# Kernel optimization log

Hardware: AMD Instinct MI355X
Metric: run time of the kernel (lower is better)

## Reference

```python
import jax, jax.numpy as jnp
import numpy as np

N_NODES = 100000
N_EDGES = 1600000
N_GRAPHS = 64
IN_CH, HID_CH, OUT_CH, N_CLS = 128, 128, 64, 2


def setup_inputs() -> dict:
    key = jax.random.key(0)
    ks = jax.random.split(key, 8)
    x = jax.random.normal(ks[0], (N_NODES, IN_CH), dtype=jnp.float32)
    edge_index = jax.random.randint(ks[1], (2, N_EDGES), 0, N_NODES)
    batch = jnp.sort(jax.random.randint(ks[2], (N_NODES,), 0, N_GRAPHS))
    glorot = lambda k, shp: jax.random.normal(k, shp, dtype=jnp.float32) / np.float32(np.sqrt(shp[0]))
    return {
        "x": x, "edge_index": edge_index, "batch": batch,
        "W1": glorot(ks[3], (IN_CH, HID_CH)), "b1": jnp.zeros((HID_CH,), jnp.float32),
        "W2": glorot(ks[4], (HID_CH, HID_CH)), "b2": jnp.zeros((HID_CH,), jnp.float32),
        "W3": glorot(ks[5], (HID_CH, OUT_CH)), "b3": jnp.zeros((OUT_CH,), jnp.float32),
        "Wfc": glorot(ks[6], (OUT_CH, N_CLS)), "bfc": jnp.zeros((N_CLS,), jnp.float32),
    }


def gcn_conv(x, src, dst, W, b):
    """PyG GCNConv: add self-loops, D^{-1/2} (A+I) D^{-1/2} (x W) + b."""
    n = x.shape[0]
    h = x @ W  # [N, out]
    # degree with self-loops: 1 + in-degree at dst
    deg = jnp.ones((n,), h.dtype).at[dst].add(1.0)
    dinv = jax.lax.rsqrt(deg)  # deg >= 1 always (self-loop)
    norm = dinv[src] * dinv[dst]  # [E]
    agg = jnp.zeros_like(h).at[dst].add(h[src] * norm[:, None])
    agg = agg + h * (dinv * dinv)[:, None]  # self-loop messages
    return agg + b


def global_mean_pool(x, batch, num_graphs):
    s = jax.ops.segment_sum(x, batch, num_segments=num_graphs)
    cnt = jax.ops.segment_sum(jnp.ones((x.shape[0],), x.dtype), batch, num_segments=num_graphs)
    return s / jnp.maximum(cnt, 1.0)[:, None]


def reference(x, edge_index, batch, W1, b1, W2, b2, W3, b3, Wfc, bfc):
    src, dst = edge_index[0], edge_index[1]
    h = jax.nn.relu(gcn_conv(x, src, dst, W1, b1))   # dropout p=0.0 (eval) -> identity
    h = jax.nn.relu(gcn_conv(h, src, dst, W2, b2))
    h = gcn_conv(h, src, dst, W3, b3)
    g = global_mean_pool(h, batch, N_GRAPHS)          # [G, OUT_CH]
    return g @ Wfc + bfc                              # [G, N_CLS]
```

## Files before the change

kernel.cpp:

```cpp
#include <hip/hip_runtime.h>
#include <hip/hip_bf16.h>


#define THREADS 256
#define BSHIFT 9
#define BSIZE 512

typedef __attribute__((ext_vector_type(8))) short short8;
typedef __attribute__((ext_vector_type(16))) float floatx16;

__device__ __forceinline__ unsigned f2bf(float f) {
    unsigned u = __float_as_uint(f);
    return (u + 0x7fffu + ((u >> 16) & 1u)) >> 16;
}

__device__ __forceinline__ void bf8_acc(uint4 v, float* ac) {
    ac[0] += __uint_as_float(v.x << 16);
    ac[1] += __uint_as_float(v.x & 0xffff0000u);
    ac[2] += __uint_as_float(v.y << 16);
    ac[3] += __uint_as_float(v.y & 0xffff0000u);
    ac[4] += __uint_as_float(v.z << 16);
    ac[5] += __uint_as_float(v.z & 0xffff0000u);
    ac[6] += __uint_as_float(v.w << 16);
    ac[7] += __uint_as_float(v.w & 0xffff0000u);
}


__global__ __launch_bounds__(512) void zero_btotal(int* btotal, int nbuck) {
    if ((int)threadIdx.x < nbuck) btotal[threadIdx.x] = 0;
}

__global__ __launch_bounds__(THREADS) void zero_f32(float* p, int n) {
    int i = blockIdx.x * THREADS + threadIdx.x;
    if (i < n) p[i] = 0.0f;
}

__global__ __launch_bounds__(THREADS) void bucket_count(const int* __restrict__ dst,
                                                        int* __restrict__ btotal,
                                                        int E, int nbuck) {
    __shared__ int cnt[BSIZE];
    for (int i = threadIdx.x; i < nbuck; i += THREADS) cnt[i] = 0;
    __syncthreads();
    for (int e = blockIdx.x * THREADS + threadIdx.x; e < E; e += gridDim.x * THREADS)
        atomicAdd(&cnt[dst[e] >> BSHIFT], 1);
    __syncthreads();
    for (int i = threadIdx.x; i < nbuck; i += THREADS) {
        int c = cnt[i];
        if (c) atomicAdd(&btotal[i], c);
    }
}

__global__ __launch_bounds__(512) void bucket_scan(const int* __restrict__ btotal,
                                                   int* __restrict__ bbase,
                                                   int* __restrict__ bcursor,
                                                   int nbuck, int E) {
    __shared__ int lds[512];
    int t = threadIdx.x;
    int v = (t < nbuck) ? btotal[t] : 0;
    lds[t] = v;
    __syncthreads();
    for (int off = 1; off < 512; off <<= 1) {
        int tv = (t >= off) ? lds[t - off] : 0;
        __syncthreads();
        lds[t] += tv;
        __syncthreads();
    }
    if (t < nbuck) {
        int excl = lds[t] - v;
        bbase[t] = excl;
        bcursor[t] = excl;
    }
    if (t == 0) bbase[nbuck] = E;
}

__global__ __launch_bounds__(THREADS) void bucket_scatter(const int* __restrict__ src,
                                                          const int* __restrict__ dst,
                                                          int* __restrict__ bcursor,
                                                          int2* __restrict__ pairs, int E) {
    __shared__ int cnt[BSIZE];
    __shared__ int base[BSIZE];
    for (int i = threadIdx.x; i < BSIZE; i += THREADS) cnt[i] = 0;
    __syncthreads();
    int e0 = blockIdx.x * 2048;
    int myb[8], myrank[8], mysrc[8], mydst[8];
#pragma unroll
    for (int j = 0; j < 8; ++j) {
        int e = e0 + j * THREADS + threadIdx.x;
        myb[j] = -1;
        if (e < E) {
            int d = dst[e];
            mysrc[j] = src[e];
            mydst[j] = d;
            myb[j] = d >> BSHIFT;
            myrank[j] = atomicAdd(&cnt[myb[j]], 1);
        }
    }
    __syncthreads();
    for (int i = threadIdx.x; i < BSIZE; i += THREADS) {
        int c = cnt[i];
        base[i] = c ? atomicAdd(&bcursor[i], c) : 0;
    }
    __syncthreads();
#pragma unroll
    for (int j = 0; j < 8; ++j)
        if (myb[j] >= 0) pairs[(size_t)base[myb[j]] + myrank[j]] = make_int2(mysrc[j], mydst[j]);
}

__global__ __launch_bounds__(512) void bucket_fill(const int2* __restrict__ pairs,
                                                   const int* __restrict__ bbase,
                                                   int* __restrict__ row_start,
                                                   float* __restrict__ dinv,
                                                   int* __restrict__ esrc,
                                                   int N, int E, int nbuck) {
    __shared__ int cnt[BSIZE];
    __shared__ int scn[BSIZE];
    int b = blockIdx.x, t = threadIdx.x;
    int s = bbase[b], e = bbase[b + 1];
    cnt[t] = 0;
    __syncthreads();
    for (int i = s + t; i < e; i += 512) atomicAdd(&cnt[pairs[i].y & (BSIZE - 1)], 1);
    __syncthreads();
    int v = cnt[t];
    scn[t] = v;
    __syncthreads();
    for (int off = 1; off < 512; off <<= 1) {
        int tv = (t >= off) ? scn[t - off] : 0;
        __syncthreads();
        scn[t] += tv;
        __syncthreads();
    }
    int excl = scn[t] - v;
    int g = (b << BSHIFT) + t;
    if (g < N) {
        row_start[g] = s + excl;
        dinv[g] = rsqrtf(1.0f + (float)v);
    }
    if (b == nbuck - 1 && t == 0) row_start[N] = E;
    scn[t] = excl;
    __syncthreads();
    for (int i = s + t; i < e; i += 512) {
        int2 p = pairs[i];
        int r = atomicAdd(&scn[p.y & (BSIZE - 1)], 1);
        esrc[s + r] = p.x;
    }
}

__global__ __launch_bounds__(THREADS) void prep_wt(const float* __restrict__ W,
                                                   uint4* __restrict__ Wtp, int C) {
    int idx = blockIdx.x * THREADS + threadIdx.x;
    if (idx >= C * 16) return;
    int c = idx >> 4, ch = idx & 15;
    unsigned r[8];
#pragma unroll
    for (int j = 0; j < 8; ++j) r[j] = f2bf(W[(size_t)(ch * 8 + j) * C + c]);
    uint4 o;
    o.x = r[0] | (r[1] << 16);
    o.y = r[2] | (r[3] << 16);
    o.z = r[4] | (r[5] << 16);
    o.w = r[6] | (r[7] << 16);
    Wtp[idx] = o;
}

template <int C, bool IN_F32>
__global__ __launch_bounds__(THREADS) void gemm_mfma(const void* __restrict__ Xin,
                                                     const uint4* __restrict__ Wt,
                                                     const float* __restrict__ dinv,
                                                     uint4* __restrict__ Hs, int n) {
    __shared__ __align__(16) char lds_raw[16384 + C * 256];
    int row0 = blockIdx.x * 64;
    int maxr = n - row0;
    if (maxr > 64) maxr = 64;
    int tid = threadIdx.x;

    if (IN_F32) {
        const float* X = (const float*)Xin;
        for (int idx = tid; idx < 1024; idx += THREADS) {
            int r = idx >> 4, c = idx & 15;
            uint4 o = make_uint4(0, 0, 0, 0);
            if (r < maxr) {
                const float* p = X + (size_t)(row0 + r) * 128 + c * 8;
                float4 a = *(const float4*)p;
                float4 b = *(const float4*)(p + 4);
                o.x = f2bf(a.x) | (f2bf(a.y) << 16);
                o.y = f2bf(a.z) | (f2bf(a.w) << 16);
                o.z = f2bf(b.x) | (f2bf(b.y) << 16);
                o.w = f2bf(b.z) | (f2bf(b.w) << 16);
            }
            *(uint4*)(lds_raw + r * 256 + ((c ^ (r & 7)) * 16)) = o;
        }
    } else {
        const uint4* X = (const uint4*)Xin;
        for (int idx = tid; idx < 1024; idx += THREADS) {
            int r = idx >> 4, c = idx & 15;
            uint4 o = (r < maxr) ? X[(size_t)(row0 + r) * 16 + c] : make_uint4(0, 0, 0, 0);
            *(uint4*)(lds_raw + r * 256 + ((c ^ (r & 7)) * 16)) = o;
        }
    }
    for (int idx = tid; idx < C * 16; idx += THREADS) {
        int cc = idx >> 4, c = idx & 15;
        *(uint4*)(lds_raw + 16384 + cc * 256 + ((c ^ (cc & 7)) * 16)) = Wt[idx];
    }
    __syncthreads();

    int wave = tid >> 6, lane = tid & 63;
    int l31 = lane & 31, half = lane >> 5;
    constexpr int MT = (C == 128) ? 2 : 1;
    int nt = wave & 1;
    int mt0 = (C == 128) ? ((wave >> 1) * 2) : (wave >> 1);
    floatx16 acc[MT];
#pragma unroll
    for (int t = 0; t < MT; ++t)
#pragma unroll
        for (int q = 0; q < 16; ++q) acc[t][q] = 0.0f;

    int xrow = nt * 32 + l31;
    const char* xbase = lds_raw + xrow * 256;
    int xsw = xrow & 7;
    const char* wbase[MT];
    int wsw[MT];
#pragma unroll
    for (int t = 0; t < MT; ++t) {
        int wrow = (mt0 + t) * 32 + l31;
        wbase[t] = lds_raw + 16384 + wrow * 256;
        wsw[t] = wrow & 7;
    }
#pragma unroll
    for (int kt = 0; kt < 8; ++kt) {
        int chunk = kt * 2 + half;
        short8 xf = *(const short8*)(xbase + ((chunk ^ xsw) * 16));
#pragma unroll
        for (int t = 0; t < MT; ++t) {
            short8 wf = *(const short8*)(wbase[t] + ((chunk ^ wsw[t]) * 16));
            acc[t] = __builtin_amdgcn_mfma_f32_32x32x16_bf16(wf, xf, acc[t], 0, 0, 0);
        }
    }
    __syncthreads();

    int node = nt * 32 + l31;
    float dv = (node < maxr) ? dinv[row0 + node] : 0.0f;
    char* outb = lds_raw;
#pragma unroll
    for (int t = 0; t < MT; ++t) {
        int cbase = (mt0 + t) * 32;
#pragma unroll
        for (int q = 0; q < 4; ++q) {
            unsigned p0 = f2bf(acc[t][q * 4 + 0] * dv) | (f2bf(acc[t][q * 4 + 1] * dv) << 16);
            unsigned p1 = f2bf(acc[t][q * 4 + 2] * dv) | (f2bf(acc[t][q * 4 + 3] * dv) << 16);
            int chunk = (cbase >> 3) + q;
            uint2 pk = make_uint2(p0, p1);
            *(uint2*)(outb + node * (C * 2) + ((chunk ^ (node & 7)) * 16) + half * 8) = pk;
        }
    }
    __syncthreads();
    constexpr int RCH = C / 8;
    for (int idx = tid; idx < maxr * RCH; idx += THREADS) {
        int r = idx / RCH, c = idx % RCH;
        uint4 v = *(const uint4*)(outb + r * (C * 2) + ((c ^ (r & 7)) * 16));
        Hs[(size_t)(row0 + r) * RCH + c] = v;
    }
}

template <int C, bool RELU>
__global__ __launch_bounds__(THREADS) void agg_kernel(const unsigned* __restrict__ Hs,
                                                      const int* __restrict__ row_start,
                                                      const int* __restrict__ esrc,
                                                      const float* __restrict__ dinv,
                                                      const float* __restrict__ bias,
                                                      unsigned* __restrict__ out, int n) {
    constexpr int LPN = C / 8;
    constexpr int NPB = THREADS / LPN;
    int node = blockIdx.x * NPB + threadIdx.x / LPN;
    int lane = threadIdx.x % LPN;
    if (node >= n) return;
    const uint4* H4 = (const uint4*)Hs;
    float di = dinv[node];
    int s = row_start[node], e = row_start[node + 1];
    float ac[8] = {0, 0, 0, 0, 0, 0, 0, 0};
    bf8_acc(H4[(size_t)node * LPN + lane], ac);
    int i = s;
    for (; i + 8 <= e; i += 8) {
        int s0 = esrc[i], s1 = esrc[i + 1], s2 = esrc[i + 2], s3 = esrc[i + 3];
        int s4 = esrc[i + 4], s5 = esrc[i + 5], s6 = esrc[i + 6], s7 = esrc[i + 7];
        uint4 v0 = H4[(size_t)s0 * LPN + lane];
        uint4 v1 = H4[(size_t)s1 * LPN + lane];
        uint4 v2 = H4[(size_t)s2 * LPN + lane];
        uint4 v3 = H4[(size_t)s3 * LPN + lane];
        uint4 v4 = H4[(size_t)s4 * LPN + lane];
        uint4 v5 = H4[(size_t)s5 * LPN + lane];
        uint4 v6 = H4[(size_t)s6 * LPN + lane];
        uint4 v7 = H4[(size_t)s7 * LPN + lane];
        bf8_acc(v0, ac); bf8_acc(v1, ac); bf8_acc(v2, ac); bf8_acc(v3, ac);
        bf8_acc(v4, ac); bf8_acc(v5, ac); bf8_acc(v6, ac); bf8_acc(v7, ac);
    }
    for (; i + 4 <= e; i += 4) {
        int s0 = esrc[i], s1 = esrc[i + 1], s2 = esrc[i + 2], s3 = esrc[i + 3];
        uint4 v0 = H4[(size_t)s0 * LPN + lane];
        uint4 v1 = H4[(size_t)s1 * LPN + lane];
        uint4 v2 = H4[(size_t)s2 * LPN + lane];
        uint4 v3 = H4[(size_t)s3 * LPN + lane];
        bf8_acc(v0, ac); bf8_acc(v1, ac); bf8_acc(v2, ac); bf8_acc(v3, ac);
    }
    for (; i < e; ++i) bf8_acc(H4[(size_t)esrc[i] * LPN + lane], ac);

    float4 b0 = ((const float4*)bias)[lane * 2];
    float4 b1 = ((const float4*)bias)[lane * 2 + 1];
    float o_[8];
    o_[0] = fmaf(di, ac[0], b0.x); o_[1] = fmaf(di, ac[1], b0.y);
    o_[2] = fmaf(di, ac[2], b0.z); o_[3] = fmaf(di, ac[3], b0.w);
    o_[4] = fmaf(di, ac[4], b1.x); o_[5] = fmaf(di, ac[5], b1.y);
    o_[6] = fmaf(di, ac[6], b1.z); o_[7] = fmaf(di, ac[7], b1.w);
    if (RELU) {
#pragma unroll
        for (int j = 0; j < 8; ++j) o_[j] = fmaxf(o_[j], 0.0f);
    }
    uint4 o;
    o.x = f2bf(o_[0]) | (f2bf(o_[1]) << 16);
    o.y = f2bf(o_[2]) | (f2bf(o_[3]) << 16);
    o.z = f2bf(o_[4]) | (f2bf(o_[5]) << 16);
    o.w = f2bf(o_[6]) | (f2bf(o_[7]) << 16);
    ((uint4*)out)[(size_t)node * LPN + lane] = o;
}

#define PCHUNK 512

__global__ __launch_bounds__(THREADS) void pool1_kernel(const unsigned* __restrict__ H3,
                                                        const int* __restrict__ batch, int n,
                                                        float* __restrict__ gsum) {
    int base = blockIdx.x * PCHUNK;
    int lane = threadIdx.x & 7;
    int sub = threadIdx.x >> 3;
    const uint4* H4 = (const uint4*)H3;
    float ac[8] = {0, 0, 0, 0, 0, 0, 0, 0};
    int cur_g = -1;
    int end = min(base + PCHUNK, n);
    for (int i = base + sub; i < end; i += 32) {
        int g = batch[i];
        if (g != cur_g) {
            if (cur_g >= 0) {
                float* p = gsum + cur_g * 64 + lane * 8;
#pragma unroll
                for (int j = 0; j < 8; ++j) atomicAdd(p + j, ac[j]);
#pragma unroll
                for (int j = 0; j < 8; ++j) ac[j] = 0.0f;
            }
            cur_g = g;
        }
        bf8_acc(H4[(size_t)i * 8 + lane], ac);
    }
    if (cur_g >= 0) {
        float* p = gsum + cur_g * 64 + lane * 8;
#pragma unroll
        for (int j = 0; j < 8; ++j) atomicAdd(p + j, ac[j]);
    }
}

__device__ __forceinline__ int dev_lower_bound(const int* a, int n, int key) {
    int lo = 0, hi = n;
    while (lo < hi) {
        int mid = (lo + hi) >> 1;
        if (a[mid] < key) lo = mid + 1;
        else hi = mid;
    }
    return lo;
}

__global__ __launch_bounds__(128) void finalize_fc(const float* __restrict__ gsum,
                                                   const int* __restrict__ batch, int n,
                                                   const float* __restrict__ Wfc,
                                                   const float* __restrict__ bfc,
                                                   float* __restrict__ out) {
    __shared__ float gm[64 * 64];
    __shared__ float cnt[64];
    int t = threadIdx.x;
    if (t < 64)
        cnt[t] = (float)(dev_lower_bound(batch, n, t + 1) - dev_lower_bound(batch, n, t));
    __syncthreads();
    for (int i = t; i < 64 * 64; i += 128) gm[i] = gsum[i] / fmaxf(cnt[i >> 6], 1.0f);
    __syncthreads();
    int g = t >> 1, cls = t & 1;
    float acc = bfc[cls];
    for (int c = 0; c < 64; ++c) acc = fmaf(gm[g * 64 + c], Wfc[c * 2 + cls], acc);
    out[g * 2 + cls] = acc;
}

extern "C" void kernel_launch(void* const* d_in, const int* in_sizes, int n_in,
                              void* d_out, int out_size, void* d_ws, size_t ws_size,
                              hipStream_t stream) {
    const float* x    = (const float*)d_in[0];
    const int*   ei   = (const int*)d_in[1];
    const int*   batch= (const int*)d_in[2];
    const float* W1   = (const float*)d_in[3];
    const float* b1   = (const float*)d_in[4];
    const float* W2   = (const float*)d_in[5];
    const float* b2   = (const float*)d_in[6];
    const float* W3   = (const float*)d_in[7];
    const float* b3   = (const float*)d_in[8];
    const float* Wfc  = (const float*)d_in[9];
    const float* bfc  = (const float*)d_in[10];
    float* out = (float*)d_out;

    const int N = in_sizes[2];
    const int E = in_sizes[1] / 2;
    const int* esrc_in = ei;
    const int* edst_in = ei + E;
    const int nbuck = (N + BSIZE - 1) >> BSHIFT;

    unsigned* bufA      = (unsigned*)d_ws;
    unsigned* bufH      = bufA + (size_t)N * 128;
    int2*     pairs     = (int2*)(bufH + (size_t)N * 64);
    int*      esrc      = (int*)(pairs + E);
    int*      row_start = esrc + E;
    float*    dinv      = (float*)(row_start + N + 1);
    int*      btotal    = (int*)(dinv + N);
    int*      bbase     = btotal + 512;
    int*      bcursor   = bbase + 513;
    float*    gsum      = (float*)(bcursor + 512);
    uint4*    Wt1       = (uint4*)(gsum + 64 * 64);
    uint4*    Wt2       = Wt1 + 2048;
    uint4*    Wt3       = Wt2 + 2048;

    prep_wt<<<8, THREADS, 0, stream>>>(W1, Wt1, 128);
    prep_wt<<<8, THREADS, 0, stream>>>(W2, Wt2, 128);
    prep_wt<<<4, THREADS, 0, stream>>>(W3, Wt3, 64);
    zero_btotal<<<1, 512, 0, stream>>>(btotal, nbuck);
    zero_f32<<<16, THREADS, 0, stream>>>(gsum, 64 * 64);
    bucket_count<<<512, THREADS, 0, stream>>>(edst_in, btotal, E, nbuck);
    bucket_scan<<<1, 512, 0, stream>>>(btotal, bbase, bcursor, nbuck, E);
    bucket_scatter<<<(E + 2047) / 2048, THREADS, 0, stream>>>(esrc_in, edst_in, bcursor, pairs, E);
    bucket_fill<<<nbuck, 512, 0, stream>>>(pairs, bbase, row_start, dinv, esrc, N, E, nbuck);

    const int GB = (N + 63) / 64;

    gemm_mfma<128, true><<<GB, THREADS, 0, stream>>>(x, Wt1, dinv, (uint4*)bufH, N);
    agg_kernel<128, true><<<(N + 15) / 16, THREADS, 0, stream>>>(bufH, row_start, esrc, dinv, b1, bufA, N);

    gemm_mfma<128, false><<<GB, THREADS, 0, stream>>>(bufA, Wt2, dinv, (uint4*)bufH, N);
    agg_kernel<128, true><<<(N + 15) / 16, THREADS, 0, stream>>>(bufH, row_start, esrc, dinv, b2, bufA, N);

    gemm_mfma<64, false><<<GB, THREADS, 0, stream>>>(bufA, Wt3, dinv, (uint4*)bufH, N);
    agg_kernel<64, false><<<(N + 31) / 32, THREADS, 0, stream>>>(bufH, row_start, esrc, dinv, b3, bufA, N);

    pool1_kernel<<<(N + PCHUNK - 1) / PCHUNK, THREADS, 0, stream>>>(bufA, batch, N, gsum);
    finalize_fc<<<1, 128, 0, stream>>>(gsum, batch, N, Wfc, bfc, out);
}
```

Measured before the change: 437.3 us.

## Fuse aggregation with next-layer GEMM, fuse final aggregation with pooling

The layer order is reassociated so each layer first aggregates the pre-scaled features and then multiplies by the weight inside one kernel, with bias, ReLU and the next dinv scaling in the GEMM epilogue. A separate prep kernel converts x to bf16 with dinv scaling. The last layer's aggregation writes straight into per-block shared-memory graph sums for mean pooling, which drops the output buffer and the pool kernel. Zeroing moves to hipMemsetAsync and the three weight-prep launches merge into one. Weights are now read from global memory per MFMA instead of being staged in LDS, and each fused block does a serial gather over 64 nodes before its GEMM.

```diff
diff --git a/kernel.cpp b/kernel.cpp
--- a/kernel.cpp
+++ b/kernel.cpp
@@ -25,15 +25,6 @@
     ac[7] += __uint_as_float(v.w & 0xffff0000u);
 }
 
-
-__global__ __launch_bounds__(512) void zero_btotal(int* btotal, int nbuck) {
-    if ((int)threadIdx.x < nbuck) btotal[threadIdx.x] = 0;
-}
-
-__global__ __launch_bounds__(THREADS) void zero_f32(float* p, int n) {
-    int i = blockIdx.x * THREADS + threadIdx.x;
-    if (i < n) p[i] = 0.0f;
-}
 
 __global__ __launch_bounds__(THREADS) void bucket_count(const int* __restrict__ dst,
                                                         int* __restrict__ btotal,
@@ -145,11 +136,8 @@
     }
 }
 
-__global__ __launch_bounds__(THREADS) void prep_wt(const float* __restrict__ W,
-                                                   uint4* __restrict__ Wtp, int C) {
-    int idx = blockIdx.x * THREADS + threadIdx.x;
-    if (idx >= C * 16) return;
-    int c = idx >> 4, ch = idx & 15;
+__device__ __forceinline__ void wt_pack(const float* W, uint4* Wtp, int C, int li) {
+    int c = li >> 4, ch = li & 15;
     unsigned r[8];
 #pragma unroll
     for (int j = 0; j < 8; ++j) r[j] = f2bf(W[(size_t)(ch * 8 + j) * C + c]);
@@ -158,79 +146,111 @@
     o.y = r[2] | (r[3] << 16);
     o.z = r[4] | (r[5] << 16);
     o.w = r[6] | (r[7] << 16);
-    Wtp[idx] = o;
-}
-
-template <int C, bool IN_F32>
-__global__ __launch_bounds__(THREADS) void gemm_mfma(const void* __restrict__ Xin,
-                                                     const uint4* __restrict__ Wt,
-                                                     const float* __restrict__ dinv,
-                                                     uint4* __restrict__ Hs, int n) {
-    __shared__ __align__(16) char lds_raw[16384 + C * 256];
+    Wtp[li] = o;
+}
+
+__global__ __launch_bounds__(THREADS) void prep_wt_all(const float* __restrict__ W1,
+                                                       const float* __restrict__ W2,
+                                                       const float* __restrict__ W3,
+                                                       uint4* __restrict__ Wt1,
+                                                       uint4* __restrict__ Wt2,
+                                                       uint4* __restrict__ Wt3) {
+    int idx = blockIdx.x * THREADS + threadIdx.x;
+    if (idx < 2048) wt_pack(W1, Wt1, 128, idx);
+    else if (idx < 4096) wt_pack(W2, Wt2, 128, idx - 2048);
+    else if (idx < 5120) wt_pack(W3, Wt3, 64, idx - 4096);
+}
+
+__global__ __launch_bounds__(THREADS) void prep_x(const float* __restrict__ x,
+                                                  const float* __restrict__ dinv,
+                                                  uint4* __restrict__ Z, int n) {
+    int idx = blockIdx.x * THREADS + threadIdx.x;
+    if (idx >= n * 16) return;
+    int r = idx >> 4, c = idx & 15;
+    float dv = dinv[r];
+    const float* p = x + (size_t)r * 128 + c * 8;
+    float4 a = *(const float4*)p;
+    float4 b = *(const float4*)(p + 4);
+    uint4 o;
+    o.x = f2bf(a.x * dv) | (f2bf(a.y * dv) << 16);
+    o.y = f2bf(a.z * dv) | (f2bf(a.w * dv) << 16);
+    o.z = f2bf(b.x * dv) | (f2bf(b.y * dv) << 16);
+    o.w = f2bf(b.z * dv) | (f2bf(b.w * dv) << 16);
+    Z[idx] = o;
+}
+
+__global__ __launch_bounds__(THREADS) void fused_layer(const uint4* __restrict__ Z,
+                                                       const uint4* __restrict__ Wt,
+                                                       const int* __restrict__ row_start,
+                                                       const int* __restrict__ esrc,
+                                                       const float* __restrict__ dinv,
+                                                       const float* __restrict__ bias,
+                                                       uint4* __restrict__ out, int n) {
+    __shared__ __align__(16) uint4 ldsX[64 * 16];
     int row0 = blockIdx.x * 64;
     int maxr = n - row0;
     if (maxr > 64) maxr = 64;
     int tid = threadIdx.x;
-
-    if (IN_F32) {
-        const float* X = (const float*)Xin;
-        for (int idx = tid; idx < 1024; idx += THREADS) {
-            int r = idx >> 4, c = idx & 15;
-            uint4 o = make_uint4(0, 0, 0, 0);
-            if (r < maxr) {
-                const float* p = X + (size_t)(row0 + r) * 128 + c * 8;
-                float4 a = *(const float4*)p;
-                float4 b = *(const float4*)(p + 4);
-                o.x = f2bf(a.x) | (f2bf(a.y) << 16);
-                o.y = f2bf(a.z) | (f2bf(a.w) << 16);
-                o.z = f2bf(b.x) | (f2bf(b.y) << 16);
-                o.w = f2bf(b.z) | (f2bf(b.w) << 16);
-            }
-            *(uint4*)(lds_raw + r * 256 + ((c ^ (r & 7)) * 16)) = o;
-        }
-    } else {
-        const uint4* X = (const uint4*)Xin;
-        for (int idx = tid; idx < 1024; idx += THREADS) {
-            int r = idx >> 4, c = idx & 15;
-            uint4 o = (r < maxr) ? X[(size_t)(row0 + r) * 16 + c] : make_uint4(0, 0, 0, 0);
-            *(uint4*)(lds_raw + r * 256 + ((c ^ (r & 7)) * 16)) = o;
-        }
-    }
-    for (int idx = tid; idx < C * 16; idx += THREADS) {
-        int cc = idx >> 4, c = idx & 15;
-        *(uint4*)(lds_raw + 16384 + cc * 256 + ((c ^ (cc & 7)) * 16)) = Wt[idx];
-    }
-    __syncthreads();
-
-    int wave = tid >> 6, lane = tid & 63;
-    int l31 = lane & 31, half = lane >> 5;
-    constexpr int MT = (C == 128) ? 2 : 1;
-    int nt = wave & 1;
-    int mt0 = (C == 128) ? ((wave >> 1) * 2) : (wave >> 1);
-    floatx16 acc[MT];
-#pragma unroll
-    for (int t = 0; t < MT; ++t)
+    int lane = tid & 15, grp = tid >> 4;
+
+    for (int round = 0; round < 4; ++round) {
+        int r = round * 16 + grp;
+        int node = row0 + r;
+        int nd = (node < n) ? node : (n - 1);
+        float ac[8] = {0, 0, 0, 0, 0, 0, 0, 0};
+        bf8_acc(Z[(size_t)nd * 16 + lane], ac);
+        int s = row_start[nd], e = row_start[nd + 1];
+        int i = s;
+        for (; i + 8 <= e; i += 8) {
+            int s0 = esrc[i], s1 = esrc[i + 1], s2 = esrc[i + 2], s3 = esrc[i + 3];
+            int s4 = esrc[i + 4], s5 = esrc[i + 5], s6 = esrc[i + 6], s7 = esrc[i + 7];
+            uint4 v0 = Z[(size_t)s0 * 16 + lane];
+            uint4 v1 = Z[(size_t)s1 * 16 + lane];
+            uint4 v2 = Z[(size_t)s2 * 16 + lane];
+            uint4 v3 = Z[(size_t)s3 * 16 + lane];
+            uint4 v4 = Z[(size_t)s4 * 16 + lane];
+            uint4 v5 = Z[(size_t)s5 * 16 + lane];
+            uint4 v6 = Z[(size_t)s6 * 16 + lane];
+            uint4 v7 = Z[(size_t)s7 * 16 + lane];
+            bf8_acc(v0, ac); bf8_acc(v1, ac); bf8_acc(v2, ac); bf8_acc(v3, ac);
+            bf8_acc(v4, ac); bf8_acc(v5, ac); bf8_acc(v6, ac); bf8_acc(v7, ac);
+        }
+        for (; i + 4 <= e; i += 4) {
+            int s0 = esrc[i], s1 = esrc[i + 1], s2 = esrc[i + 2], s3 = esrc[i + 3];
+            uint4 v0 = Z[(size_t)s0 * 16 + lane];
+            uint4 v1 = Z[(size_t)s1 * 16 + lane];
+            uint4 v2 = Z[(size_t)s2 * 16 + lane];
+            uint4 v3 = Z[(size_t)s3 * 16 + lane];
+            bf8_acc(v0, ac); bf8_acc(v1, ac); bf8_acc(v2, ac); bf8_acc(v3, ac);
+        }
+        for (; i < e; ++i) bf8_acc(Z[(size_t)esrc[i] * 16 + lane], ac);
+        float dv = dinv[nd];
+        uint4 o;
+        o.x = f2bf(ac[0] * dv) | (f2bf(ac[1] * dv) << 16);
+        o.y = f2bf(ac[2] * dv) | (f2bf(ac[3] * dv) << 16);
+        o.z = f2bf(ac[4] * dv) | (f2bf(ac[5] * dv) << 16);
+        o.w = f2bf(ac[6] * dv) | (f2bf(ac[7] * dv) << 16);
+        ldsX[r * 16 + (lane ^ (r & 7))] = o;
+    }
+    __syncthreads();
+
+    int l = tid & 63, wv = tid >> 6;
+    int l31 = l & 31, half = l >> 5;
+    int nt = wv & 1, mt0 = (wv >> 1) * 2;
+    floatx16 acc[2];
+#pragma unroll
+    for (int t = 0; t < 2; ++t)
 #pragma unroll
         for (int q = 0; q < 16; ++q) acc[t][q] = 0.0f;
-
-    int xrow = nt * 32 + l31;
-    const char* xbase = lds_raw + xrow * 256;
-    int xsw = xrow & 7;
-    const char* wbase[MT];
-    int wsw[MT];
-#pragma unroll
-    for (int t = 0; t < MT; ++t) {
-        int wrow = (mt0 + t) * 32 + l31;
-        wbase[t] = lds_raw + 16384 + wrow * 256;
-        wsw[t] = wrow & 7;
-    }
+    int xrow = nt * 32 + l31, xsw = xrow & 7;
 #pragma unroll
     for (int kt = 0; kt < 8; ++kt) {
         int chunk = kt * 2 + half;
-        short8 xf = *(const short8*)(xbase + ((chunk ^ xsw) * 16));
-#pragma unroll
-        for (int t = 0; t < MT; ++t) {
-            short8 wf = *(const short8*)(wbase[t] + ((chunk ^ wsw[t]) * 16));
+        short8 xf = *(const short8*)&ldsX[xrow * 16 + (chunk ^ xsw)];
+#pragma unroll
+        for (int t = 0; t < 2; ++t) {
+            int c = (mt0 + t) * 32 + l31;
+            short8 wf = *(const short8*)&Wt[c * 16 + chunk];
             acc[t] = __builtin_amdgcn_mfma_f32_32x32x16_bf16(wf, xf, acc[t], 0, 0, 0);
         }
     }
@@ -238,119 +258,147 @@
 
     int node = nt * 32 + l31;
     float dv = (node < maxr) ? dinv[row0 + node] : 0.0f;
-    char* outb = lds_raw;
-#pragma unroll
-    for (int t = 0; t < MT; ++t) {
-        int cbase = (mt0 + t) * 32;
+    char* outb = (char*)ldsX;
+#pragma unroll
+    for (int t = 0; t < 2; ++t) {
+        int cb = (mt0 + t) * 32;
 #pragma unroll
         for (int q = 0; q < 4; ++q) {
-            unsigned p0 = f2bf(acc[t][q * 4 + 0] * dv) | (f2bf(acc[t][q * 4 + 1] * dv) << 16);
-            unsigned p1 = f2bf(acc[t][q * 4 + 2] * dv) | (f2bf(acc[t][q * 4 + 3] * dv) << 16);
-            int chunk = (cbase >> 3) + q;
-            uint2 pk = make_uint2(p0, p1);
-            *(uint2*)(outb + node * (C * 2) + ((chunk ^ (node & 7)) * 16) + half * 8) = pk;
-        }
-    }
-    __syncthreads();
-    constexpr int RCH = C / 8;
-    for (int idx = tid; idx < maxr * RCH; idx += THREADS) {
-        int r = idx / RCH, c = idx % RCH;
-        uint4 v = *(const uint4*)(outb + r * (C * 2) + ((c ^ (r & 7)) * 16));
-        Hs[(size_t)(row0 + r) * RCH + c] = v;
-    }
-}
-
-template <int C, bool RELU>
-__global__ __launch_bounds__(THREADS) void agg_kernel(const unsigned* __restrict__ Hs,
-                                                      const int* __restrict__ row_start,
-                                                      const int* __restrict__ esrc,
-                                                      const float* __restrict__ dinv,
-                                                      const float* __restrict__ bias,
-                                                      unsigned* __restrict__ out, int n) {
-    constexpr int LPN = C / 8;
-    constexpr int NPB = THREADS / LPN;
-    int node = blockIdx.x * NPB + threadIdx.x / LPN;
-    int lane = threadIdx.x % LPN;
-    if (node >= n) return;
-    const uint4* H4 = (const uint4*)Hs;
-    float di = dinv[node];
-    int s = row_start[node], e = row_start[node + 1];
-    float ac[8] = {0, 0, 0, 0, 0, 0, 0, 0};
-    bf8_acc(H4[(size_t)node * LPN + lane], ac);
-    int i = s;
-    for (; i + 8 <= e; i += 8) {
-        int s0 = esrc[i], s1 = esrc[i + 1], s2 = esrc[i + 2], s3 = esrc[i + 3];
-        int s4 = esrc[i + 4], s5 = esrc[i + 5], s6 = esrc[i + 6], s7 = esrc[i + 7];
-        uint4 v0 = H4[(size_t)s0 * LPN + lane];
-        uint4 v1 = H4[(size_t)s1 * LPN + lane];
-        uint4 v2 = H4[(size_t)s2 * LPN + lane];
-        uint4 v3 = H4[(size_t)s3 * LPN + lane];
-        uint4 v4 = H4[(size_t)s4 * LPN + lane];
-        uint4 v5 = H4[(size_t)s5 * LPN + lane];
-        uint4 v6 = H4[(size_t)s6 * LPN + lane];
-        uint4 v7 = H4[(size_t)s7 * LPN + lane];
-        bf8_acc(v0, ac); bf8_acc(v1, ac); bf8_acc(v2, ac); bf8_acc(v3, ac);
-        bf8_acc(v4, ac); bf8_acc(v5, ac); bf8_acc(v6, ac); bf8_acc(v7, ac);
-    }
-    for (; i + 4 <= e; i += 4) {
-        int s0 = esrc[i], s1 = esrc[i + 1], s2 = esrc[i + 2], s3 = esrc[i + 3];
-        uint4 v0 = H4[(size_t)s0 * LPN + lane];
-        uint4 v1 = H4[(size_t)s1 * LPN + lane];
-        uint4 v2 = H4[(size_t)s2 * LPN + lane];
-        uint4 v3 = H4[(size_t)s3 * LPN + lane];
-        bf8_acc(v0, ac); bf8_acc(v1, ac); bf8_acc(v2, ac); bf8_acc(v3, ac);
-    }
-    for (; i < e; ++i) bf8_acc(H4[(size_t)esrc[i] * LPN + lane], ac);
-
-    float4 b0 = ((const float4*)bias)[lane * 2];
-    float4 b1 = ((const float4*)bias)[lane * 2 + 1];
-    float o_[8];
-    o_[0] = fmaf(di, ac[0], b0.x); o_[1] = fmaf(di, ac[1], b0.y);
-    o_[2] = fmaf(di, ac[2], b0.z); o_[3] = fmaf(di, ac[3], b0.w);
-    o_[4] = fmaf(di, ac[4], b1.x); o_[5] = fmaf(di, ac[5], b1.y);
-    o_[6] = fmaf(di, ac[6], b1.z); o_[7] = fmaf(di, ac[7], b1.w);
-    if (RELU) {
-#pragma unroll
-        for (int j = 0; j < 8; ++j) o_[j] = fmaxf(o_[j], 0.0f);
-    }
-    uint4 o;
-    o.x = f2bf(o_[0]) | (f2bf(o_[1]) << 16);
-    o.y = f2bf(o_[2]) | (f2bf(o_[3]) << 16);
-    o.z = f2bf(o_[4]) | (f2bf(o_[5]) << 16);
-    o.w = f2bf(o_[6]) | (f2bf(o_[7]) << 16);
-    ((uint4*)out)[(size_t)node * LPN + lane] = o;
-}
-
-#define PCHUNK 512
-
-__global__ __launch_bounds__(THREADS) void pool1_kernel(const unsigned* __restrict__ H3,
-                                                        const int* __restrict__ batch, int n,
-                                                        float* __restrict__ gsum) {
-    int base = blockIdx.x * PCHUNK;
-    int lane = threadIdx.x & 7;
-    int sub = threadIdx.x >> 3;
-    const uint4* H4 = (const uint4*)H3;
-    float ac[8] = {0, 0, 0, 0, 0, 0, 0, 0};
-    int cur_g = -1;
-    int end = min(base + PCHUNK, n);
-    for (int i = base + sub; i < end; i += 32) {
-        int g = batch[i];
-        if (g != cur_g) {
-            if (cur_g >= 0) {
-                float* p = gsum + cur_g * 64 + lane * 8;
-#pragma unroll
-                for (int j = 0; j < 8; ++j) atomicAdd(p + j, ac[j]);
-#pragma unroll
-                for (int j = 0; j < 8; ++j) ac[j] = 0.0f;
+            float v[4];
+#pragma unroll
+            for (int m = 0; m < 4; ++m) {
+                int ch = cb + 8 * q + 4 * half + m;
+                float x_ = acc[t][q * 4 + m] + bias[ch];
+                x_ = fmaxf(x_, 0.0f);
+                v[m] = x_ * dv;
             }
-            cur_g = g;
-        }
-        bf8_acc(H4[(size_t)i * 8 + lane], ac);
-    }
-    if (cur_g >= 0) {
-        float* p = gsum + cur_g * 64 + lane * 8;
-#pragma unroll
-        for (int j = 0; j < 8; ++j) atomicAdd(p + j, ac[j]);
+            uint2 pk = make_uint2(f2bf(v[0]) | (f2bf(v[1]) << 16),
+                                  f2bf(v[2]) | (f2bf(v[3]) << 16));
+            int chunk = (cb >> 3) + q;
+            *(uint2*)(outb + node * 256 + ((chunk ^ (node & 7)) * 16) + half * 8) = pk;
+        }
+    }
+    __syncthreads();
+    for (int idx = tid; idx < maxr * 16; idx += THREADS) {
+        int r = idx >> 4, c = idx & 15;
+        out[(size_t)(row0 + r) * 16 + c] = *(uint4*)(outb + r * 256 + ((c ^ (r & 7)) * 16));
+    }
+}
+
+__global__ __launch_bounds__(THREADS) void gemm3(const uint4* __restrict__ Z,
+                                                 const uint4* __restrict__ Wt,
+                                                 uint4* __restrict__ out, int n) {
+    __shared__ __align__(16) uint4 ldsX[64 * 16];
+    int row0 = blockIdx.x * 64;
+    int maxr = n - row0;
+    if (maxr > 64) maxr = 64;
+    int tid = threadIdx.x;
+    for (int idx = tid; idx < 1024; idx += THREADS) {
+        int r = idx >> 4, c = idx & 15;
+        uint4 o = (r < maxr) ? Z[(size_t)(row0 + r) * 16 + c] : make_uint4(0, 0, 0, 0);
+        ldsX[r * 16 + (c ^ (r & 7))] = o;
+    }
+    __syncthreads();
+    int l = tid & 63, wv = tid >> 6;
+    int l31 = l & 31, half = l >> 5;
+    int nt = wv & 1, mt = wv >> 1;
+    floatx16 acc;
+#pragma unroll
+    for (int q = 0; q < 16; ++q) acc[q] = 0.0f;
+    int xrow = nt * 32 + l31, xsw = xrow & 7;
+#pragma unroll
+    for (int kt = 0; kt < 8; ++kt) {
+        int chunk = kt * 2 + half;
+        short8 xf = *(const short8*)&ldsX[xrow * 16 + (chunk ^ xsw)];
+        int c = mt * 32 + l31;
+        short8 wf = *(const short8*)&Wt[c * 16 + chunk];
+        acc = __builtin_amdgcn_mfma_f32_32x32x16_bf16(wf, xf, acc, 0, 0, 0);
+    }
+    __syncthreads();
+    int node = nt * 32 + l31;
+    char* outb = (char*)ldsX;
+    int cb = mt * 32;
+#pragma unroll
+    for (int q = 0; q < 4; ++q) {
+        uint2 pk = make_uint2(f2bf(acc[q * 4 + 0]) | (f2bf(acc[q * 4 + 1]) << 16),
+                              f2bf(acc[q * 4 + 2]) | (f2bf(acc[q * 4 + 3]) << 16));
+        int chunk = (cb >> 3) + q;
+        *(uint2*)(outb + node * 128 + ((chunk ^ (node & 7)) * 16) + half * 8) = pk;
+    }
+    __syncthreads();
+    for (int idx = tid; idx < maxr * 8; idx += THREADS) {
+        int r = idx >> 3, c = idx & 7;
+        out[(size_t)(row0 + r) * 8 + c] = *(uint4*)(outb + r * 128 + ((c ^ (r & 7)) * 16));
+    }
+}
+
+__global__ __launch_bounds__(THREADS) void agg_pool(const uint4* __restrict__ Ps,
+                                                    const int* __restrict__ row_start,
+                                                    const int* __restrict__ esrc,
+                                                    const float* __restrict__ dinv,
+                                                    const float* __restrict__ bias,
+                                                    const int* __restrict__ batch,
+                                                    float* __restrict__ gsum, int n) {
+    __shared__ float gpart[32][65];
+    __shared__ int used[32];
+    int tid = threadIdx.x;
+    int lane = tid & 7, grp = tid >> 3;
+    int node = blockIdx.x * 32 + grp;
+    if (tid < 32) used[tid] = 0;
+    for (int idx = tid; idx < 2048; idx += THREADS) gpart[idx >> 6][idx & 63] = 0.0f;
+    __syncthreads();
+    int gmin = batch[blockIdx.x * 32];
+    if (node < n) {
+        float ac[8] = {0, 0, 0, 0, 0, 0, 0, 0};
+        bf8_acc(Ps[(size_t)node * 8 + lane], ac);
+        int s = row_start[node], e = row_start[node + 1];
+        int i = s;
+        for (; i + 8 <= e; i += 8) {
+            int s0 = esrc[i], s1 = esrc[i + 1], s2 = esrc[i + 2], s3 = esrc[i + 3];
+            int s4 = esrc[i + 4], s5 = esrc[i + 5], s6 = esrc[i + 6], s7 = esrc[i + 7];
+            uint4 v0 = Ps[(size_t)s0 * 8 + lane];
+            uint4 v1 = Ps[(size_t)s1 * 8 + lane];
+            uint4 v2 = Ps[(size_t)s2 * 8 + lane];
+            uint4 v3 = Ps[(size_t)s3 * 8 + lane];
+            uint4 v4 = Ps[(size_t)s4 * 8 + lane];
+            uint4 v5 = Ps[(size_t)s5 * 8 + lane];
+            uint4 v6 = Ps[(size_t)s6 * 8 + lane];
+            uint4 v7 = Ps[(size_t)s7 * 8 + lane];
+            bf8_acc(v0, ac); bf8_acc(v1, ac); bf8_acc(v2, ac); bf8_acc(v3, ac);
+            bf8_acc(v4, ac); bf8_acc(v5, ac); bf8_acc(v6, ac); bf8_acc(v7, ac);
+        }
+        for (; i + 4 <= e; i += 4) {
+            int s0 = esrc[i], s1 = esrc[i + 1], s2 = esrc[i + 2], s3 = esrc[i + 3];
+            uint4 v0 = Ps[(size_t)s0 * 8 + lane];
+            uint4 v1 = Ps[(size_t)s1 * 8 + lane];
+            uint4 v2 = Ps[(size_t)s2 * 8 + lane];
+            uint4 v3 = Ps[(size_t)s3 * 8 + lane];
+            bf8_acc(v0, ac); bf8_acc(v1, ac); bf8_acc(v2, ac); bf8_acc(v3, ac);
+        }
+        for (; i < e; ++i) bf8_acc(Ps[(size_t)esrc[i] * 8 + lane], ac);
+        float dv = dinv[node];
+        float4 b0 = ((const float4*)bias)[lane * 2];
+        float4 b1 = ((const float4*)bias)[lane * 2 + 1];
+        float h[8];
+        h[0] = fmaf(dv, ac[0], b0.x); h[1] = fmaf(dv, ac[1], b0.y);
+        h[2] = fmaf(dv, ac[2], b0.z); h[3] = fmaf(dv, ac[3], b0.w);
+        h[4] = fmaf(dv, ac[4], b1.x); h[5] = fmaf(dv, ac[5], b1.y);
+        h[6] = fmaf(dv, ac[6], b1.z); h[7] = fmaf(dv, ac[7], b1.w);
+        int g = batch[node];
+        int slot = g - gmin;
+        if (slot < 32) {
+            if (lane == 0) used[slot] = 1;
+#pragma unroll
+            for (int j = 0; j < 8; ++j) atomicAdd(&gpart[slot][lane * 8 + j], h[j]);
+        } else {
+#pragma unroll
+            for (int j = 0; j < 8; ++j) atomicAdd(&gsum[(size_t)g * 64 + lane * 8 + j], h[j]);
+        }
+    }
+    __syncthreads();
+    for (int idx = tid; idx < 2048; idx += THREADS) {
+        int s = idx >> 6, ch = idx & 63;
+        if (used[s]) atomicAdd(&gsum[(size_t)(gmin + s) * 64 + ch], gpart[s][ch]);
     }
 }
 
@@ -405,41 +453,36 @@
     const int* edst_in = ei + E;
     const int nbuck = (N + BSIZE - 1) >> BSHIFT;
 
-    unsigned* bufA      = (unsigned*)d_ws;
-    unsigned* bufH      = bufA + (size_t)N * 128;
-    int2*     pairs     = (int2*)(bufH + (size_t)N * 64);
-    int*      esrc      = (int*)(pairs + E);
-    int*      row_start = esrc + E;
-    float*    dinv      = (float*)(row_start + N + 1);
-    int*      btotal    = (int*)(dinv + N);
-    int*      bbase     = btotal + 512;
-    int*      bcursor   = bbase + 513;
-    float*    gsum      = (float*)(bcursor + 512);
-    uint4*    Wt1       = (uint4*)(gsum + 64 * 64);
-    uint4*    Wt2       = Wt1 + 2048;
-    uint4*    Wt3       = Wt2 + 2048;
-
-    prep_wt<<<8, THREADS, 0, stream>>>(W1, Wt1, 128);
-    prep_wt<<<8, THREADS, 0, stream>>>(W2, Wt2, 128);
-    prep_wt<<<4, THREADS, 0, stream>>>(W3, Wt3, 64);
-    zero_btotal<<<1, 512, 0, stream>>>(btotal, nbuck);
-    zero_f32<<<16, THREADS, 0, stream>>>(gsum, 64 * 64);
+    uint4* bufA      = (uint4*)d_ws;
+    uint4* bufB      = bufA + (size_t)N * 16;
+    uint4* bufC      = bufB + (size_t)N * 16;
+    int2*  pairs     = (int2*)(bufC + (size_t)N * 8);
+    int*   esrc      = (int*)(pairs + E);
+    int*   row_start = esrc + E;
+    float* dinv      = (float*)(row_start + N + 1);
+    int*   btotal    = (int*)(dinv + N);
+    int*   bbase     = btotal + 512;
+    int*   bcursor   = bbase + 513;
+    float* gsum      = (float*)(bcursor + 512);
+    uint4* Wt1       = (uint4*)(gsum + 64 * 64 + 2);
+    uint4* Wt2       = Wt1 + 2048;
+    uint4* Wt3       = Wt2 + 2048;
+
+    hipMemsetAsync(btotal, 0, 512 * sizeof(int), stream);
+    hipMemsetAsync(gsum, 0, 64 * 64 * sizeof(float), stream);
     bucket_count<<<512, THREADS, 0, stream>>>(edst_in, btotal, E, nbuck);
     bucket_scan<<<1, 512, 0, stream>>>(btotal, bbase, bcursor, nbuck, E);
     bucket_scatter<<<(E + 2047) / 2048, THREADS, 0, stream>>>(esrc_in, edst_in, bcursor, pairs, E);
     bucket_fill<<<nbuck, 512, 0, stream>>>(pairs, bbase, row_start, dinv, esrc, N, E, nbuck);
+    prep_wt_all<<<20, THREADS, 0, stream>>>(W1, W2, W3, Wt1, Wt2, Wt3);
+    prep_x<<<(N * 16 + THREADS - 1) / THREADS, THREADS, 0, stream>>>(x, dinv, bufA, N);
 
     const int GB = (N + 63) / 64;
 
-    gemm_mfma<128, true><<<GB, THREADS, 0, stream>>>(x, Wt1, dinv, (uint4*)bufH, N);
-    agg_kernel<128, true><<<(N + 15) / 16, THREADS, 0, stream>>>(bufH, row_start, esrc, dinv, b1, bufA, N);
-
-    gemm_mfma<128, false><<<GB, THREADS, 0, stream>>>(bufA, Wt2, dinv, (uint4*)bufH, N);
-    agg_kernel<128, true><<<(N + 15) / 16, THREADS, 0, stream>>>(bufH, row_start, esrc, dinv, b2, bufA, N);
-
-    gemm_mfma<64, false><<<GB, THREADS, 0, stream>>>(bufA, Wt3, dinv, (uint4*)bufH, N);
-    agg_kernel<64, false><<<(N + 31) / 32, THREADS, 0, stream>>>(bufH, row_start, esrc, dinv, b3, bufA, N);
-
-    pool1_kernel<<<(N + PCHUNK - 1) / PCHUNK, THREADS, 0, stream>>>(bufA, batch, N, gsum);
+    fused_layer<<<GB, THREADS, 0, stream>>>(bufA, Wt1, row_start, esrc, dinv, b1, bufB, N);
+    fused_layer<<<GB, THREADS, 0, stream>>>(bufB, Wt2, row_start, esrc, dinv, b2, bufA, N);
+    gemm3<<<GB, THREADS, 0, stream>>>(bufA, Wt3, bufC, N);
+    agg_pool<<<(N + 31) / 32, THREADS, 0, stream>>>(bufC, row_start, esrc, dinv, b3, batch, gsum, N);
+
     finalize_fc<<<1, 128, 0, stream>>>(gsum, batch, N, Wfc, bfc, out);
 }
```

After: 440.7 us. No clear change (+0.8%).
